# Kernel optimization log

Measured on AMD Instinct MI355X. Metric: run time of the kernel, lower is better.

The kernel has to match this reference:

```python
import jax, jax.numpy as jnp
import numpy as np
import math

D = 512      # input_size == hidden_size
TAU = 4      # length of att/spatial lists
N = 16384    # tokens (batch*H*W)

def setup_inputs() -> dict:
    key = jax.random.key(0)
    ks = jax.random.split(key, 16)
    s = 1.0 / math.sqrt(D)
    return {
        "T_t": jax.random.normal(ks[0], (N, D), jnp.float32),
        "S_t": jax.random.normal(ks[1], (N, D), jnp.float32),
        "t_att": jax.random.normal(ks[2], (TAU, N, D), jnp.float32),
        "s_att": jax.random.normal(ks[3], (TAU, N, D), jnp.float32),
        "t_spatial": jax.random.normal(ks[4], (TAU, N, D), jnp.float32),
        "s_spatial": jax.random.normal(ks[5], (TAU, N, D), jnp.float32),
        # fl_t: Linear(D, 3D); fl_t_next: Linear(D, D); same for s
        "W_t": jax.random.uniform(ks[6], (3 * D, D), jnp.float32, -s, s),
        "b_t": jax.random.uniform(ks[7], (3 * D,), jnp.float32, -s, s),
        "W_tn": jax.random.uniform(ks[8], (D, D), jnp.float32, -s, s),
        "b_tn": jax.random.uniform(ks[9], (D,), jnp.float32, -s, s),
        "W_s": jax.random.uniform(ks[10], (3 * D, D), jnp.float32, -s, s),
        "b_s": jax.random.uniform(ks[11], (3 * D,), jnp.float32, -s, s),
        "W_sn": jax.random.uniform(ks[12], (D, D), jnp.float32, -s, s),
        "b_sn": jax.random.uniform(ks[13], (D,), jnp.float32, -s, s),
    }

def reference(T_t, S_t, t_att, s_att, t_spatial, s_spatial,
              W_t, b_t, W_tn, b_tn, W_s, b_s, W_sn, b_sn):
    d = T_t.shape[-1]
    scale = 1.0 / jnp.sqrt(jnp.asarray(d, T_t.dtype))
    s_next = S_t @ W_sn.T + b_sn          # [N, D]
    t_next = T_t @ W_tn.T + b_tn          # [N, D]

    # trend weights: dot-product along feature dim, softmax over tau axis
    w_s = jax.nn.softmax(jnp.einsum('knd,nd->kn', s_att, s_next) * scale, axis=0)
    w_t = jax.nn.softmax(jnp.einsum('knd,nd->kn', t_spatial, t_next) * scale, axis=0)
    T_trend = jnp.einsum('knd,kn->nd', t_att, w_s)      # [N, D]
    S_trend = jnp.einsum('knd,kn->nd', s_spatial, w_t)  # [N, D]

    t_gate = jax.nn.sigmoid(t_next)
    s_gate = jax.nn.sigmoid(s_next)
    T_fusion = T_t * t_gate + (1.0 - t_gate) * T_trend
    S_fusion = S_t * s_gate + (1.0 - s_gate) * S_trend

    T_concat = T_fusion @ W_t.T + b_t     # [N, 3D]
    S_concat = S_fusion @ W_s.T + b_s
    t_g, t_t, t_s = jnp.split(T_concat, 3, axis=1)
    s_g, s_t, s_s = jnp.split(S_concat, 3, axis=1)
    T_gate = jax.nn.sigmoid(t_g)
    S_gate = jax.nn.sigmoid(s_g)
    T_new = T_gate * t_t + (1.0 - T_gate) * s_t
    S_new = S_gate * s_s + (1.0 - S_gate) * t_s
    return T_new, S_new
```

## Files before the change

kernel.cpp:

```cpp
#include <hip/hip_runtime.h>

#define NTOK 16384
#define DIM 512
#define NTAU 4

typedef __attribute__((ext_vector_type(4))) float f32x4;
typedef __attribute__((ext_vector_type(8))) short bf16x8;
typedef __attribute__((ext_vector_type(4))) unsigned short u16x4;
typedef __attribute__((ext_vector_type(8))) unsigned short u16x8;
typedef unsigned int u32;

__device__ inline unsigned short f2bf(float f) {
    union { float f; unsigned int u; } v; v.f = f;
    unsigned int u = v.u + 0x7FFFu + ((v.u >> 16) & 1u);
    return (unsigned short)(u >> 16);
}

__device__ inline void bf8_to_f32(u16x8 h, f32x4& a, f32x4& b) {
    union { unsigned int u; float f; } t;
#pragma unroll
    for (int e = 0; e < 4; e++) { t.u = ((unsigned int)h[e]) << 16; a[e] = t.f; }
#pragma unroll
    for (int e = 0; e < 4; e++) { t.u = ((unsigned int)h[4 + e]) << 16; b[e] = t.f; }
}

#define NTLOAD4(p) __builtin_nontemporal_load((const f32x4*)(p))

__device__ __forceinline__ void gload16(const void* g, void* l) {
    __builtin_amdgcn_global_load_lds((const __attribute__((address_space(1))) u32*)g,
                                     (__attribute__((address_space(3))) u32*)l, 16, 0, 0);
}

__global__ void convert_all(const float* __restrict__ a, const float* __restrict__ b,
                            const float* __restrict__ c, const float* __restrict__ d,
                            unsigned short* __restrict__ oa, unsigned short* __restrict__ ob,
                            unsigned short* __restrict__ oc, unsigned short* __restrict__ od) {
    int i = blockIdx.x * 256 + threadIdx.x;
    const float* s; unsigned short* t; int off;
    if (i < 65536)       { s = a; t = oa; off = i; }
    else if (i < 131072) { s = b; t = ob; off = i - 65536; }
    else if (i < 327680) { s = c; t = oc; off = i - 131072; }
    else                 { s = d; t = od; off = i - 327680; }
    f32x4 v = ((const f32x4*)s)[off];
    u16x4 o;
    o[0] = f2bf(v[0]); o[1] = f2bf(v[1]); o[2] = f2bf(v[2]); o[3] = f2bf(v[3]);
    ((u16x4*)t)[off] = o;
}

__global__ __launch_bounds__(256, 2) void gemm_next2(
    const float* __restrict__ T_t, const float* __restrict__ S_t,
    const unsigned short* __restrict__ Wtn, const unsigned short* __restrict__ Wsn,
    const float* __restrict__ btn, const float* __restrict__ bsn,
    unsigned short* __restrict__ t_next, unsigned short* __restrict__ s_next)
{
    __shared__ unsigned short lA[128][40];
    __shared__ unsigned short lB[128][40];
    const int tid = threadIdx.x;
    const int id = blockIdx.x;
    const int xcd = id & 7;
    const int rest = id >> 3;
    const int mat = rest & 1;
    const int idx = rest >> 1;
    const float* A = mat ? S_t : T_t;
    const unsigned short* W = mat ? Wsn : Wtn;
    const float* bias = mat ? bsn : btn;
    unsigned short* out = mat ? s_next : t_next;
    const int m0 = (xcd * 16 + (idx >> 2)) * 128;
    const int n0 = (idx & 3) * 128;
    const int lane = tid & 63;
    const int w = tid >> 6;
    const int wr = w >> 1, wc = w & 1;

    f32x4 acc[4][4];
#pragma unroll
    for (int i = 0; i < 4; i++)
#pragma unroll
        for (int j = 0; j < 4; j++) acc[i][j] = (f32x4){0.f, 0.f, 0.f, 0.f};

    const int arow = tid >> 3;
    const int acol = (tid & 7) * 4;
    const int brow = tid >> 2;
    const int bcol = (tid & 3) * 8;

    for (int k0 = 0; k0 < DIM; k0 += 32) {
#pragma unroll
        for (int i = 0; i < 4; i++) {
            int r = arow + 32 * i;
            f32x4 v = *(const f32x4*)(A + (size_t)(m0 + r) * DIM + k0 + acol);
            u16x4 o;
            o[0] = f2bf(v[0]); o[1] = f2bf(v[1]); o[2] = f2bf(v[2]); o[3] = f2bf(v[3]);
            *(u16x4*)&lA[r][acol] = o;
        }
#pragma unroll
        for (int i = 0; i < 2; i++) {
            int r = brow + 64 * i;
            u16x8 v = *(const u16x8*)(W + (size_t)(n0 + r) * DIM + k0 + bcol);
            *(u16x8*)&lB[r][bcol] = v;
        }
        __syncthreads();

        bf16x8 af[4], bfr[4];
#pragma unroll
        for (int i = 0; i < 4; i++)
            af[i] = *(const bf16x8*)&lA[wr * 64 + i * 16 + (lane & 15)][(lane >> 4) * 8];
#pragma unroll
        for (int j = 0; j < 4; j++)
            bfr[j] = *(const bf16x8*)&lB[wc * 64 + j * 16 + (lane & 15)][(lane >> 4) * 8];
#pragma unroll
        for (int i = 0; i < 4; i++)
#pragma unroll
            for (int j = 0; j < 4; j++)
                acc[i][j] = __builtin_amdgcn_mfma_f32_16x16x32_bf16(af[i], bfr[j], acc[i][j], 0, 0, 0);
        __syncthreads();
    }

#pragma unroll
    for (int j = 0; j < 4; j++) {
        int n = n0 + wc * 64 + j * 16 + (lane & 15);
        float bv = bias[n];
#pragma unroll
        for (int i = 0; i < 4; i++) {
            int mbase = m0 + wr * 64 + i * 16 + (lane >> 4) * 4;
#pragma unroll
            for (int r = 0; r < 4; r++)
                out[(size_t)(mbase + r) * DIM + n] = f2bf(acc[i][j][r] + bv);
        }
    }
}

__global__ __launch_bounds__(256) void dots_kernel(
    const float* __restrict__ s_att, const float* __restrict__ t_spatial,
    const unsigned short* __restrict__ t_next, const unsigned short* __restrict__ s_next,
    float* __restrict__ w_all)
{
    const int lane = threadIdx.x & 63;
    const int id = blockIdx.x;
    const int n = (id & 7) * 2048 + (id >> 3) * 4 + (threadIdx.x >> 6);
    const int c = lane * 8;
    const size_t rb = (size_t)n * DIM + c;
    const float scale = 0.04419417382415922f;

    f32x4 tn_a, tn_b, sn_a, sn_b;
    bf8_to_f32(*(const u16x8*)(t_next + rb), tn_a, tn_b);
    bf8_to_f32(*(const u16x8*)(s_next + rb), sn_a, sn_b);

    float dws[NTAU], dwt[NTAU];
#pragma unroll
    for (int k = 0; k < NTAU; k++) {
        const size_t kb = ((size_t)k * NTOK + n) * DIM + c;
        f32x4 a0 = NTLOAD4(s_att + kb);
        f32x4 a1 = NTLOAD4(s_att + kb + 4);
        f32x4 b0 = NTLOAD4(t_spatial + kb);
        f32x4 b1 = NTLOAD4(t_spatial + kb + 4);
        dws[k] = a0[0]*sn_a[0]+a0[1]*sn_a[1]+a0[2]*sn_a[2]+a0[3]*sn_a[3]
               + a1[0]*sn_b[0]+a1[1]*sn_b[1]+a1[2]*sn_b[2]+a1[3]*sn_b[3];
        dwt[k] = b0[0]*tn_a[0]+b0[1]*tn_a[1]+b0[2]*tn_a[2]+b0[3]*tn_a[3]
               + b1[0]*tn_b[0]+b1[1]*tn_b[1]+b1[2]*tn_b[2]+b1[3]*tn_b[3];
    }
#pragma unroll
    for (int k = 0; k < NTAU; k++) {
        float v = dws[k];
#pragma unroll
        for (int off = 32; off; off >>= 1) v += __shfl_xor(v, off);
        dws[k] = v * scale;
        float u = dwt[k];
#pragma unroll
        for (int off = 32; off; off >>= 1) u += __shfl_xor(u, off);
        dwt[k] = u * scale;
    }

    float ms = fmaxf(fmaxf(dws[0], dws[1]), fmaxf(dws[2], dws[3]));
    float mt = fmaxf(fmaxf(dwt[0], dwt[1]), fmaxf(dwt[2], dwt[3]));
    f32x4 wsv, wtv;
    float ssum = 0.f, tsum = 0.f;
#pragma unroll
    for (int k = 0; k < NTAU; k++) {
        wsv[k] = __expf(dws[k] - ms); ssum += wsv[k];
        wtv[k] = __expf(dwt[k] - mt); tsum += wtv[k];
    }
    float rs = 1.f / ssum, rt = 1.f / tsum;
#pragma unroll
    for (int k = 0; k < NTAU; k++) { wsv[k] *= rs; wtv[k] *= rt; }

    if (lane == 0) {
        *(f32x4*)(w_all + (size_t)n * 8)     = wsv;
        *(f32x4*)(w_all + (size_t)n * 8 + 4) = wtv;
    }
}

__global__ __launch_bounds__(256) void fusion_kernel(
    const float* __restrict__ T_t, const float* __restrict__ S_t,
    const float* __restrict__ t_att, const float* __restrict__ s_spatial,
    const unsigned short* __restrict__ t_next, const unsigned short* __restrict__ s_next,
    const float* __restrict__ w_all,
    unsigned short* __restrict__ Tf, unsigned short* __restrict__ Sf)
{
    const int lane = threadIdx.x & 63;
    const int id = blockIdx.x;
    const int n = (id & 7) * 2048 + (id >> 3) * 4 + (threadIdx.x >> 6);
    const int c = lane * 8;
    const size_t rb = (size_t)n * DIM + c;

    f32x4 wsv = *(const f32x4*)(w_all + (size_t)n * 8);
    f32x4 wtv = *(const f32x4*)(w_all + (size_t)n * 8 + 4);

    f32x4 Tta = {0,0,0,0}, Ttb = {0,0,0,0}, Sta = {0,0,0,0}, Stb = {0,0,0,0};
#pragma unroll
    for (int k = 0; k < NTAU; k++) {
        const size_t kb = ((size_t)k * NTOK + n) * DIM + c;
        f32x4 ta = NTLOAD4(t_att + kb);
        f32x4 tb = NTLOAD4(t_att + kb + 4);
        f32x4 sa = NTLOAD4(s_spatial + kb);
        f32x4 sb = NTLOAD4(s_spatial + kb + 4);
        float wk = wsv[k], vk = wtv[k];
#pragma unroll
        for (int e = 0; e < 4; e++) {
            Tta[e] += wk * ta[e]; Ttb[e] += wk * tb[e];
            Sta[e] += vk * sa[e]; Stb[e] += vk * sb[e];
        }
    }

    f32x4 tn_a, tn_b, sn_a, sn_b;
    bf8_to_f32(*(const u16x8*)(t_next + rb), tn_a, tn_b);
    bf8_to_f32(*(const u16x8*)(s_next + rb), sn_a, sn_b);
    f32x4 Ta = NTLOAD4(T_t + rb);
    f32x4 Tb = NTLOAD4(T_t + rb + 4);
    f32x4 Sa = NTLOAD4(S_t + rb);
    f32x4 Sb = NTLOAD4(S_t + rb + 4);

    u16x8 oT, oS;
#pragma unroll
    for (int e = 0; e < 4; e++) {
        float gt_a = 1.f / (1.f + __expf(-tn_a[e]));
        float gt_b = 1.f / (1.f + __expf(-tn_b[e]));
        float gs_a = 1.f / (1.f + __expf(-sn_a[e]));
        float gs_b = 1.f / (1.f + __expf(-sn_b[e]));
        oT[e]     = f2bf(Ta[e] * gt_a + (1.f - gt_a) * Tta[e]);
        oT[4 + e] = f2bf(Tb[e] * gt_b + (1.f - gt_b) * Ttb[e]);
        oS[e]     = f2bf(Sa[e] * gs_a + (1.f - gs_a) * Sta[e]);
        oS[4 + e] = f2bf(Sb[e] * gs_b + (1.f - gs_b) * Stb[e]);
    }
    *(u16x8*)(Tf + rb) = oT;
    *(u16x8*)(Sf + rb) = oS;
}

__global__ __launch_bounds__(512, 2) void gemm_final(
    const unsigned short* __restrict__ Tf, const unsigned short* __restrict__ Sf,
    const unsigned short* __restrict__ Wt, const unsigned short* __restrict__ Ws,
    const float* __restrict__ bt, const float* __restrict__ bs,
    float* __restrict__ out)
{
    __shared__ __align__(16) unsigned short lT[2][128][32];
    __shared__ __align__(16) unsigned short lS[2][128][32];
    __shared__ __align__(16) unsigned short lW[2][384][32];
    const int tid = threadIdx.x;
    const int id = blockIdx.x;
    const int xcd = id & 7;
    const int idx = id >> 3;
    const int m0 = (xcd * 16 + (idx >> 3)) * 128;
    const int j0 = (idx & 7) * 64;
    const int lane = tid & 63;
    const int w = tid >> 6;
    const int wr = w & 1;
    const int wjc = w >> 1;

    f32x4 acc[6][4];
#pragma unroll
    for (int g = 0; g < 6; g++)
#pragma unroll
        for (int i = 0; i < 4; i++) acc[g][i] = (f32x4){0.f, 0.f, 0.f, 0.f};

    const int srow = lane >> 2;
    const int sg   = lane & 3;

    auto stage = [&](int buf, int kt) {
        const int k0 = kt * 32;
#pragma unroll
        for (int i = 0; i < 5; i++) {
            const int ch = w * 5 + i;
            if (ch < 8) {
                const int row = ch * 16 + srow;
                const int lg = sg ^ ((row >> 1) & 3);
                gload16(Tf + (size_t)(m0 + row) * DIM + k0 + lg * 8, &lT[buf][ch * 16][0]);
            } else if (ch < 16) {
                const int row = (ch - 8) * 16 + srow;
                const int lg = sg ^ ((row >> 1) & 3);
                gload16(Sf + (size_t)(m0 + row) * DIM + k0 + lg * 8, &lS[buf][(ch - 8) * 16][0]);
            } else {
                const int rb = (ch - 16) * 16;
                const int r = rb + srow;
                const int lg = sg ^ ((r >> 1) & 3);
                const int g = r >> 6;
                const unsigned short* src = (g < 3) ? Wt : Ws;
                const int wrow = (g < 3 ? g : g - 3) * DIM + j0 + (r & 63);
                gload16(src + (size_t)wrow * DIM + k0 + lg * 8, &lW[buf][rb][0]);
            }
        }
    };

    stage(0, 0);
    __syncthreads();

    int cur = 0;
    for (int kt = 0; kt < 16; ++kt) {
        if (kt < 15) stage(cur ^ 1, kt + 1);

        bf16x8 aT[4], aS[4];
#pragma unroll
        for (int i = 0; i < 4; i++) {
            const int row = wr * 64 + i * 16 + (lane & 15);
            const int pg = (lane >> 4) ^ ((row >> 1) & 3);
            aT[i] = *(const bf16x8*)&lT[cur][row][pg * 8];
            aS[i] = *(const bf16x8*)&lS[cur][row][pg * 8];
        }
#pragma unroll
        for (int g = 0; g < 6; g++) {
            const int r = g * 64 + wjc * 16 + (lane & 15);
            const int pg = (lane >> 4) ^ ((r >> 1) & 3);
            bf16x8 bw = *(const bf16x8*)&lW[cur][r][pg * 8];
#pragma unroll
            for (int i = 0; i < 4; i++)
                acc[g][i] = __builtin_amdgcn_mfma_f32_16x16x32_bf16(
                    (g < 3) ? aT[i] : aS[i], bw, acc[g][i], 0, 0, 0);
        }
        __syncthreads();
        cur ^= 1;
    }

    const int j = j0 + wjc * 16 + (lane & 15);
    const float btg = bt[j], btt = bt[512 + j], bts = bt[1024 + j];
    const float bsg = bs[j], bst = bs[512 + j], bss = bs[1024 + j];
#pragma unroll
    for (int i = 0; i < 4; i++) {
        int mbase = m0 + wr * 64 + i * 16 + (lane >> 4) * 4;
#pragma unroll
        for (int r = 0; r < 4; r++) {
            float TG = acc[0][i][r] + btg;
            float TT = acc[1][i][r] + btt;
            float TS = acc[2][i][r] + bts;
            float SG = acc[3][i][r] + bsg;
            float ST = acc[4][i][r] + bst;
            float SS = acc[5][i][r] + bss;
            float gT = 1.f / (1.f + __expf(-TG));
            float gS = 1.f / (1.f + __expf(-SG));
            size_t m = (size_t)(mbase + r);
            out[m * DIM + j] = gT * TT + (1.f - gT) * ST;
            out[(size_t)NTOK * DIM + m * DIM + j] = gS * SS + (1.f - gS) * TS;
        }
    }
}

extern "C" void kernel_launch(void* const* d_in, const int* in_sizes, int n_in,
                              void* d_out, int out_size, void* d_ws, size_t ws_size,
                              hipStream_t stream) {
    const float* T_t       = (const float*)d_in[0];
    const float* S_t       = (const float*)d_in[1];
    const float* t_att     = (const float*)d_in[2];
    const float* s_att     = (const float*)d_in[3];
    const float* t_spatial = (const float*)d_in[4];
    const float* s_spatial = (const float*)d_in[5];
    const float* W_t  = (const float*)d_in[6];
    const float* b_t  = (const float*)d_in[7];
    const float* W_tn = (const float*)d_in[8];
    const float* b_tn = (const float*)d_in[9];
    const float* W_s  = (const float*)d_in[10];
    const float* b_s  = (const float*)d_in[11];
    const float* W_sn = (const float*)d_in[12];
    const float* b_sn = (const float*)d_in[13];
    float* out = (float*)d_out;

    char* ws = (char*)d_ws;
    unsigned short* t_next = (unsigned short*)(ws + 0);
    unsigned short* s_next = (unsigned short*)(ws + 16777216);
    unsigned short* Tf     = (unsigned short*)(ws + 33554432);
    unsigned short* Sf     = (unsigned short*)(ws + 50331648);
    unsigned short* Wtn_b  = (unsigned short*)(ws + 67108864);
    unsigned short* Wsn_b  = (unsigned short*)(ws + 67633152);
    unsigned short* Wt_b   = (unsigned short*)(ws + 68157440);
    unsigned short* Ws_b   = (unsigned short*)(ws + 69730304);
    float*          w_all  = (float*)(ws + 71303168);

    convert_all<<<2048, 256, 0, stream>>>(W_tn, W_sn, W_t, W_s,
                                          Wtn_b, Wsn_b, Wt_b, Ws_b);

    gemm_next2<<<1024, 256, 0, stream>>>(T_t, S_t, Wtn_b, Wsn_b, b_tn, b_sn,
                                         t_next, s_next);

    dots_kernel<<<4096, 256, 0, stream>>>(s_att, t_spatial, t_next, s_next, w_all);

    fusion_kernel<<<4096, 256, 0, stream>>>(T_t, S_t, t_att, s_spatial,
                                            t_next, s_next, w_all, Tf, Sf);

    gemm_final<<<1024, 512, 0, stream>>>(Tf, Sf, Wt_b, Ws_b, b_t, b_s, out);
}
```

Before: 289.0 us.

## Split final GEMM tile by T/S side per wave and exchange cross terms via LDS

After: 290.4 us. About the same (+0.5%).

```diff
diff --git a/kernel.cpp b/kernel.cpp
--- a/kernel.cpp
+++ b/kernel.cpp
@@ -244,31 +244,34 @@
     *(u16x8*)(Sf + rb) = oS;
 }
 
-__global__ __launch_bounds__(512, 2) void gemm_final(
+__global__ __launch_bounds__(256, 2) void gemm_final(
     const unsigned short* __restrict__ Tf, const unsigned short* __restrict__ Sf,
     const unsigned short* __restrict__ Wt, const unsigned short* __restrict__ Ws,
     const float* __restrict__ bt, const float* __restrict__ bs,
     float* __restrict__ out)
 {
-    __shared__ __align__(16) unsigned short lT[2][128][32];
-    __shared__ __align__(16) unsigned short lS[2][128][32];
-    __shared__ __align__(16) unsigned short lW[2][384][32];
+    __shared__ __align__(16) unsigned char smem[57344];
+    auto lT = (unsigned short (*)[128][32])(smem);
+    auto lS = (unsigned short (*)[128][32])(smem + 16384);
+    auto lW = (unsigned short (*)[192][32])(smem + 32768);
+    auto ex = (float (*)[16][132])(smem);
+
     const int tid = threadIdx.x;
     const int id = blockIdx.x;
     const int xcd = id & 7;
     const int idx = id >> 3;
-    const int m0 = (xcd * 16 + (idx >> 3)) * 128;
-    const int j0 = (idx & 7) * 64;
+    const int m0 = (xcd * 16 + (idx >> 4)) * 128;
+    const int j0 = (idx & 15) * 32;
     const int lane = tid & 63;
     const int w = tid >> 6;
-    const int wr = w & 1;
-    const int wjc = w >> 1;
-
-    f32x4 acc[6][4];
-#pragma unroll
-    for (int g = 0; g < 6; g++)
-#pragma unroll
-        for (int i = 0; i < 4; i++) acc[g][i] = (f32x4){0.f, 0.f, 0.f, 0.f};
+    const int side = w >> 1;
+    const int jq = w & 1;
+
+    f32x4 acc[3][8];
+#pragma unroll
+    for (int g = 0; g < 3; g++)
+#pragma unroll
+        for (int i = 0; i < 8; i++) acc[g][i] = (f32x4){0.f, 0.f, 0.f, 0.f};
 
     const int srow = lane >> 2;
     const int sg   = lane & 3;
@@ -276,8 +279,8 @@
     auto stage = [&](int buf, int kt) {
         const int k0 = kt * 32;
 #pragma unroll
-        for (int i = 0; i < 5; i++) {
-            const int ch = w * 5 + i;
+        for (int i = 0; i < 7; i++) {
+            const int ch = w * 7 + i;
             if (ch < 8) {
                 const int row = ch * 16 + srow;
                 const int lg = sg ^ ((row >> 1) & 3);
@@ -287,13 +290,13 @@
                 const int lg = sg ^ ((row >> 1) & 3);
                 gload16(Sf + (size_t)(m0 + row) * DIM + k0 + lg * 8, &lS[buf][(ch - 8) * 16][0]);
             } else {
-                const int rb = (ch - 16) * 16;
-                const int r = rb + srow;
+                const int rbse = (ch - 16) * 16;
+                const int r = rbse + srow;
                 const int lg = sg ^ ((r >> 1) & 3);
-                const int g = r >> 6;
+                const int g = r >> 5;
                 const unsigned short* src = (g < 3) ? Wt : Ws;
-                const int wrow = (g < 3 ? g : g - 3) * DIM + j0 + (r & 63);
-                gload16(src + (size_t)wrow * DIM + k0 + lg * 8, &lW[buf][rb][0]);
+                const int wrow = (g < 3 ? g : g - 3) * DIM + j0 + (r & 31);
+                gload16(src + (size_t)wrow * DIM + k0 + lg * 8, &lW[buf][rbse][0]);
             }
         }
     };
@@ -305,47 +308,58 @@
     for (int kt = 0; kt < 16; ++kt) {
         if (kt < 15) stage(cur ^ 1, kt + 1);
 
-        bf16x8 aT[4], aS[4];
-#pragma unroll
-        for (int i = 0; i < 4; i++) {
-            const int row = wr * 64 + i * 16 + (lane & 15);
+        unsigned short (*lA)[32] = side ? lS[cur] : lT[cur];
+        bf16x8 ax[8], bw[3];
+#pragma unroll
+        for (int i = 0; i < 8; i++) {
+            const int row = i * 16 + (lane & 15);
             const int pg = (lane >> 4) ^ ((row >> 1) & 3);
-            aT[i] = *(const bf16x8*)&lT[cur][row][pg * 8];
-            aS[i] = *(const bf16x8*)&lS[cur][row][pg * 8];
-        }
-#pragma unroll
-        for (int g = 0; g < 6; g++) {
-            const int r = g * 64 + wjc * 16 + (lane & 15);
+            ax[i] = *(const bf16x8*)&lA[row][pg * 8];
+        }
+#pragma unroll
+        for (int g = 0; g < 3; g++) {
+            const int r = (side * 3 + g) * 32 + jq * 16 + (lane & 15);
             const int pg = (lane >> 4) ^ ((r >> 1) & 3);
-            bf16x8 bw = *(const bf16x8*)&lW[cur][r][pg * 8];
-#pragma unroll
-            for (int i = 0; i < 4; i++)
-                acc[g][i] = __builtin_amdgcn_mfma_f32_16x16x32_bf16(
-                    (g < 3) ? aT[i] : aS[i], bw, acc[g][i], 0, 0, 0);
-        }
+            bw[g] = *(const bf16x8*)&lW[cur][r][pg * 8];
+        }
+#pragma unroll
+        for (int g = 0; g < 3; g++)
+#pragma unroll
+            for (int i = 0; i < 8; i++)
+                acc[g][i] = __builtin_amdgcn_mfma_f32_16x16x32_bf16(ax[i], bw[g], acc[g][i], 0, 0, 0);
+
         __syncthreads();
         cur ^= 1;
     }
 
-    const int j = j0 + wjc * 16 + (lane & 15);
-    const float btg = bt[j], btt = bt[512 + j], bts = bt[1024 + j];
-    const float bsg = bs[j], bst = bs[512 + j], bss = bs[1024 + j];
-#pragma unroll
-    for (int i = 0; i < 4; i++) {
-        int mbase = m0 + wr * 64 + i * 16 + (lane >> 4) * 4;
+    const int j = j0 + jq * 16 + (lane & 15);
+    const float b0 = side ? bs[j]        : bt[j];
+    const float b1 = side ? bs[512 + j]  : bt[512 + j];
+    const float b2 = side ? bs[1024 + j] : bt[1024 + j];
+
+    const int col = lane & 15;
+#pragma unroll
+    for (int i = 0; i < 8; i++) {
+        const int rowb = i * 16 + (lane >> 4) * 4;
+        f32x4 v = side ? acc[1][i] : acc[2][i];
+        const float bb = side ? b1 : b2;
+        v[0] += bb; v[1] += bb; v[2] += bb; v[3] += bb;
+        *(f32x4*)&ex[w][col][rowb] = v;
+    }
+    __syncthreads();
+
+    float* obase = out + (side ? (size_t)NTOK * DIM : 0);
+    const float bown = side ? b2 : b1;
+    const int gown = side ? 2 : 1;
+#pragma unroll
+    for (int i = 0; i < 8; i++) {
+        const int rowb = i * 16 + (lane >> 4) * 4;
+        f32x4 oth = *(const f32x4*)&ex[w ^ 2][col][rowb];
 #pragma unroll
         for (int r = 0; r < 4; r++) {
-            float TG = acc[0][i][r] + btg;
-            float TT = acc[1][i][r] + btt;
-            float TS = acc[2][i][r] + bts;
-            float SG = acc[3][i][r] + bsg;
-            float ST = acc[4][i][r] + bst;
-            float SS = acc[5][i][r] + bss;
-            float gT = 1.f / (1.f + __expf(-TG));
-            float gS = 1.f / (1.f + __expf(-SG));
-            size_t m = (size_t)(mbase + r);
-            out[m * DIM + j] = gT * TT + (1.f - gT) * ST;
-            out[(size_t)NTOK * DIM + m * DIM + j] = gS * SS + (1.f - gS) * TS;
+            const float gate = 1.f / (1.f + __expf(-(acc[0][i][r] + b0)));
+            const float own = acc[gown][i][r] + bown;
+            obase[(size_t)(m0 + rowb + r) * DIM + j] = gate * own + (1.f - gate) * oth[r];
         }
     }
 }
@@ -391,5 +405,5 @@
     fusion_kernel<<<4096, 256, 0, stream>>>(T_t, S_t, t_att, s_spatial,
                                             t_next, s_next, w_all, Tf, Sf);
 
-    gemm_final<<<1024, 512, 0, stream>>>(Tf, Sf, Wt_b, Ws_b, b_t, b_s, out);
-}
+    gemm_final<<<2048, 256, 0, stream>>>(Tf, Sf, Wt_b, Ws_b, b_t, b_s, out);
+}
```
